# Kernel tuning notes

Hardware: AMD Instinct MI355X
Metric: run time of the kernel (lower is better)

Reference implementation:

```python
import jax, jax.numpy as jnp
import numpy as np

CR = 64                      # cond_repeat
DILS = tuple(2 ** i for _ in range(2) for i in range(10))  # 2 blocks x 10 layers
Q_ZERO = 128


def setup_inputs() -> dict:
    key = jax.random.key(0)
    B, C, TE = 8, 64, 8          # batch, cond channels, encoding timesteps
    R, S, Q = 128, 128, 256      # residual, skip, classes
    L = len(DILS)
    ks = jax.random.split(key, 12)
    sc = 0.1
    return {
        "encodings": jax.random.normal(ks[0], (B, C, TE), jnp.float32),
        "first_w": jax.random.normal(ks[1], (R, 1, 2), jnp.float32) * sc,
        "first_b": jnp.zeros((R,), jnp.float32),
        "causal_w": jax.random.normal(ks[2], (L, 2 * R, R, 2), jnp.float32) * sc,
        "causal_b": jnp.zeros((L, 2 * R), jnp.float32),
        "cond_w": jax.random.normal(ks[3], (L, 2 * R, C), jnp.float32) * sc,
        "cond_b": jnp.zeros((L, 2 * R), jnp.float32),
        "res_w": jax.random.normal(ks[4], (L, R, R), jnp.float32) * sc,
        "res_b": jnp.zeros((L, R), jnp.float32),
        "skip_w": jax.random.normal(ks[5], (L, S, R), jnp.float32) * sc,
        "skip_b": jnp.zeros((L, S), jnp.float32),
        "skipc_w": jax.random.normal(ks[6], (S, R), jnp.float32) * sc,
        "skipc_b": jnp.zeros((S,), jnp.float32),
        "fc_w": jax.random.normal(ks[7], (S, S), jnp.float32) * sc,
        "fc_b": jnp.zeros((S,), jnp.float32),
        "condf_w": jax.random.normal(ks[8], (S, C), jnp.float32) * sc,
        "condf_b": jnp.zeros((S,), jnp.float32),
        "logits_w": jax.random.normal(ks[9], (Q, S), jnp.float32) * sc,
        "logits_b": jnp.zeros((Q,), jnp.float32),
    }


def _generate(encodings, first_w, first_b, causal_w, causal_b, cond_w, cond_b,
              res_w, res_b, skip_w, skip_b, skipc_w, skipc_b, fc_w, fc_b,
              condf_w, condf_b, logits_w, logits_b):
    B = encodings.shape[0]
    R = res_w.shape[1]
    T = encodings.shape[2] * CR

    # ring buffers emulate QueuedConv1d (queue length = dilation, zero-initialized)
    buf_first0 = jnp.zeros((B, 1), jnp.float32)
    bufs0 = tuple(jnp.zeros((B, d, R), jnp.float32) for d in DILS)
    sample0 = jnp.full((B,), Q_ZERO, jnp.int32)

    def step(carry, t):
        sample, buf_first, bufs = carry
        x = sample.astype(jnp.float32) / 255.0 - 0.5                      # [B]
        c = jax.lax.dynamic_index_in_dim(encodings, t // CR, axis=2,
                                         keepdims=False)                  # [B,C]
        # first causal conv (1 -> R, kernel 2): tap0 on delayed sample, tap1 on current
        prev0 = buf_first[:, 0]
        buf_first = buf_first.at[:, 0].set(x)
        res = (prev0[:, None] * first_w[None, :, 0, 0]
               + x[:, None] * first_w[None, :, 0, 1] + first_b)           # [B,R]
        skip = res @ skipc_w.T + skipc_b                                  # [B,S]
        new_bufs = []
        for l, d in enumerate(DILS):
            idx = jnp.mod(t, d)
            prev = jax.lax.dynamic_index_in_dim(bufs[l], idx, axis=1, keepdims=False)
            new_bufs.append(jax.lax.dynamic_update_index_in_dim(bufs[l], res, idx, axis=1))
            z = (prev @ causal_w[l, :, :, 0].T + res @ causal_w[l, :, :, 1].T
                 + causal_b[l] + c @ cond_w[l].T + cond_b[l])             # [B,2R]
            gate, out = jnp.split(z, 2, axis=1)
            h = jax.nn.sigmoid(gate) * jnp.tanh(out)                      # [B,R]
            res = res + h @ res_w[l].T + res_b[l]
            skip = skip + h @ skip_w[l].T + skip_b[l]
        s = jax.nn.relu(skip) @ fc_w.T + fc_b + c @ condf_w.T + condf_b
        logits = jax.nn.relu(s) @ logits_w.T + logits_b                   # [B,Q]
        sample = jnp.argmax(logits, axis=1).astype(jnp.int32)             # 'max' sampling
        return (sample, buf_first, tuple(new_bufs)), (sample, logits)

    _, (samples, logits) = jax.lax.scan(step, (sample0, buf_first0, bufs0),
                                        jnp.arange(T))
    return samples, logits  # [T,B] int32, [T,B,Q] float32


def reference(encodings, first_w, first_b, causal_w, causal_b, cond_w, cond_b,
              res_w, res_b, skip_w, skip_b, skipc_w, skipc_b, fc_w, fc_b,
              condf_w, condf_b, logits_w, logits_b):
    return _generate(encodings, first_w, first_b, causal_w, causal_b, cond_w, cond_b,
                     res_w, res_b, skip_w, skip_b, skipc_w, skipc_b, fc_w, fc_b,
                     condf_w, condf_b, logits_w, logits_b)
```

## Files before the change

### kernel.cpp

```cpp
#include <hip/hip_runtime.h>
#include <math.h>

#define BB 8
#define TT 512
#define LL 20
#define NBLK 64
#define NTHR 256

typedef float f4 __attribute__((ext_vector_type(4)));
typedef unsigned long long ull;

__constant__ int c_dil[LL] = {1,2,4,8,16,32,64,128,256,512,
                              1,2,4,8,16,32,64,128,256,512};
__constant__ int c_roff[LL] = {-1,0,4096,12288,28672,61440,126976,258048,520192,1044480,
                               2093056,2095104,2099200,2107392,2123776,2156544,
                               2222080,2353152,2615296,3139584};

constexpr size_t OFF_RING = 0;
constexpr size_t OFF_X    = 4188160;

#define P_WC     0
#define P_TB     0
#define P_F      20480
#define P_CZ0    30208
#define P_KC     32256
#define P_WST    32512
#define P_WF0    33024
#define P_WF1    33152
#define P_FB     33280
#define P_CONDZ  33408
#define P_SFC    34048
#define P_RESB   34064
#define P_SKIPB  34104
#define P_ZB     34144
#define P_LOGB   34224
#define P_SKC    34228
#define P_XS     34234
#define P_SL     34258
#define P_SKACC  34290
#define P_R2     34306
#define P_CF     34322
#define P_PREVF  34852
#define P_HF     35908
#define P_RESF   38020
#define POOL_FL  40132

__device__ __forceinline__ f4 ldx(const f4* p) {
    f4 r;
    asm volatile("global_load_dwordx4 %0, %1, off sc0 sc1\n\ts_waitcnt vmcnt(0)"
                 : "=v"(r) : "v"(p) : "memory");
    return r;
}
__device__ __forceinline__ void ldx2(const f4* p0, const f4* p1, f4& a, f4& b) {
    asm volatile("global_load_dwordx4 %0, %2, off sc0 sc1\n\t"
                 "global_load_dwordx4 %1, %3, off sc0 sc1\n\t"
                 "s_waitcnt vmcnt(0)"
                 : "=&v"(a), "=&v"(b) : "v"(p0), "v"(p1) : "memory");
}
__device__ __forceinline__ void ld4x(const f4* a0, const f4* a1, const f4* a2, const f4* a3,
                                     f4& r0, f4& r1, f4& r2, f4& r3) {
    asm volatile("global_load_dwordx4 %0, %4, off sc0 sc1\n\t"
                 "global_load_dwordx4 %1, %5, off sc0 sc1\n\t"
                 "global_load_dwordx4 %2, %6, off sc0 sc1\n\t"
                 "global_load_dwordx4 %3, %7, off sc0 sc1\n\t"
                 "s_waitcnt vmcnt(0)"
                 : "=&v"(r0), "=&v"(r1), "=&v"(r2), "=&v"(r3)
                 : "v"(a0), "v"(a1), "v"(a2), "v"(a3) : "memory");
}
__device__ __forceinline__ void stx(f4* p, f4 v) {
    asm volatile("global_store_dwordx4 %0, %1, off sc0 sc1"
                 :: "v"(p), "v"(v) : "memory");
}
__device__ __forceinline__ void spin(const f4* p, int e, f4& a) {
    while (__float_as_int(a.w) != e) a = ldx(p);
}

__device__ __forceinline__ void pub2(f4* slot, int J, int q, float v0, float v1, int e) {
    f4 v; v.x = v0; v.y = v1; v.z = 0.f; v.w = __int_as_float(e);
    stx(slot + J*8 + q, v);
}
__device__ __forceinline__ void scat2(float* dst, f4 v, int idx, bool dorelu) {
    int Jb = idx >> 3, q = idx & 7;
    float x = v.x, y = v.y;
    if (dorelu) { x = fmaxf(x, 0.f); y = fmaxf(y, 0.f); }
    if (q < 4) {
        dst[(2*q)*132 + 2*Jb]     = x;
        dst[(2*q+1)*132 + 2*Jb]   = y;
    } else {
        dst[(2*q-8)*132 + 2*Jb+1] = x;
        dst[(2*q-7)*132 + 2*Jb+1] = y;
    }
}
__device__ __forceinline__ void consume(const f4* slot, int e, float* dst, bool dorelu) {
    int m = threadIdx.x;
    const f4 *p0 = slot + m, *p1 = slot + 256 + m;
    f4 a, b;
    ldx2(p0, p1, a, b);
    spin(p0, e, a);
    spin(p1, e, b);
    scat2(dst, a, m, dorelu);
    scat2(dst, b, m + 256, dorelu);
}
__device__ __forceinline__ void consume_pair(const f4* sR, int eR, float* dR,
                                             const f4* sH, int eH, float* dH) {
    int m = threadIdx.x;
    const f4 *pra = sR + m, *prb = sR + 256 + m, *pha = sH + m, *phb = sH + 256 + m;
    f4 ra, rb, ha, hb;
    ld4x(pra, prb, pha, phb, ra, rb, ha, hb);
    spin(pra, eR, ra);
    spin(prb, eR, rb);
    scat2(dR, ra, m, false);
    scat2(dR, rb, m + 256, false);
    spin(pha, eH, ha);
    spin(phb, eH, hb);
    scat2(dH, ha, m, false);
    scat2(dH, hb, m + 256, false);
}

__global__ __launch_bounds__(NTHR, 1) void wn_gen(
    const float* __restrict__ enc,
    const float* __restrict__ first_w,  const float* __restrict__ first_b,
    const float* __restrict__ causal_w, const float* __restrict__ causal_b,
    const float* __restrict__ cond_w,   const float* __restrict__ cond_b,
    const float* __restrict__ res_w,    const float* __restrict__ res_b,
    const float* __restrict__ skip_w,   const float* __restrict__ skip_b,
    const float* __restrict__ skipc_w,  const float* __restrict__ skipc_b,
    const float* __restrict__ fc_w,     const float* __restrict__ fc_b,
    const float* __restrict__ condf_w,  const float* __restrict__ condf_b,
    const float* __restrict__ logits_w, const float* __restrict__ logits_b,
    float* __restrict__ wsf, float* __restrict__ out)
{
    extern __shared__ float pool[];
    const int tid = threadIdx.x;
    const int J = blockIdx.x;
    float* ring = wsf + OFF_RING;
    f4* xb = (f4*)(wsf + OFF_X);

    for (int m = 1024 + tid; m < 20480; m += NTHR) {
        int l = m >> 10, rem = m & 1023, g = rem >> 8, i = rem & 255;
        int grow = (g < 2) ? (2*J + g) : (128 + 2*J + (g - 2));
        int col = i & 127, k = i >> 7;
        pool[P_WC + m] = causal_w[((size_t)(l*256 + grow)*128 + col)*2 + k];
    }
    if (tid < 128) {
        pool[P_WF0 + tid] = first_w[2*tid];
        pool[P_WF1 + tid] = first_w[2*tid + 1];
        pool[P_FB + tid]  = first_b[tid];
    }
    if (tid < 40) {
        int l = tid >> 1, r = tid & 1;
        pool[P_RESB + tid]  = res_b[l*128 + 2*J + r];
        pool[P_SKIPB + tid] = skip_b[l*128 + 2*J + r];
    }
    if (tid < 4) pool[P_LOGB + tid] = logits_b[4*J + tid];
    if (tid < 8) {
        pool[P_XS + tid]      = 128.f/255.f - 0.5f;
        pool[P_XS + 8 + tid]  = 0.f;
        pool[P_XS + 16 + tid] = 0.f;
    }
    float wl[16], wfc[16];
    {
        int g = (tid >> 3) & 3, k = tid & 7;
        #pragma unroll
        for (int i = 0; i < 16; ++i)
            wl[i] = logits_w[(size_t)(4*J + g)*128 + k + 8*i];
        int r2 = (tid >> 6) & 1;
        #pragma unroll
        for (int i = 0; i < 16; ++i)
            wfc[i] = fc_w[(size_t)(2*J + r2)*128 + k + 8*i];
    }
    __syncthreads();

    for (int l = 0; l < 19; ++l) {
        for (int m = tid; m < 512; m += NTHR) {
            int g = m >> 7, j = m & 127;
            const float* w1 = pool + P_WC + ((l+1)*4 + g)*256 + 128;
            const float* rw = res_w + (size_t)l*128*128 + j;
            float acc = 0.f;
            #pragma unroll 8
            for (int i = 0; i < 128; ++i) acc += w1[i] * rw[(size_t)i*128];
            pool[P_F + (l*4 + g)*128 + j] = acc;
        }
    }
    if (tid < 80) {
        int l = tid >> 2, g = tid & 3;
        float acc = 0.f;
        if (l >= 1) {
            const float* w1 = pool + P_WC + (l*4 + g)*256 + 128;
            for (int i = 0; i < 128; ++i) acc += w1[i] * res_b[(l-1)*128 + i];
        }
        pool[P_ZB + tid] = acc;
    }
    {
        int grow = tid;
        const float* cw0 = causal_w + (size_t)grow*256;
        float u = 0.f, c1 = 0.f, a0 = 0.f, kp = 0.f, kc = 0.f;
        for (int j = 0; j < 128; ++j) {
            float w0 = cw0[2*j], w1 = cw0[2*j + 1];
            float f0 = pool[P_WF0 + j], f1 = pool[P_WF1 + j], fbv = pool[P_FB + j];
            u  += w0*f0;  c1 += w0*f1 + w1*f0;  a0 += w1*f1;
            kp += w0*fbv; kc += w1*fbv;
        }
        pool[P_TB + grow*4 + 0] = u;
        pool[P_TB + grow*4 + 1] = c1;
        pool[P_TB + grow*4 + 2] = a0;
        pool[P_TB + grow*4 + 3] = kp;
        pool[P_KC + grow]       = kc;
    }
    if (tid < 2) {
        const float* wr = skipc_w + (size_t)(2*J + tid)*128;
        float sk = skipc_b[2*J + tid], sa = 0.f, sb = 0.f;
        for (int j = 0; j < 128; ++j) {
            sk += wr[j]*pool[P_FB + j];
            sa += wr[j]*pool[P_WF0 + j];
            sb += wr[j]*pool[P_WF1 + j];
        }
        pool[P_SKC + tid*3 + 0] = sk;
        pool[P_SKC + tid*3 + 1] = sa;
        pool[P_SKC + tid*3 + 2] = sb;
    }
    __syncthreads();

    int e = 0;
    int er_pending = 0;
    int esk = 0;

    const int w = tid >> 6, lane = tid & 63;

    for (int t = 0; t < TT; ++t) {
        if ((t & 63) == 0) {
            int te = t >> 6;
            for (int m = tid; m < 512; m += NTHR) {
                int b = m >> 6, j = m & 63;
                pool[P_CF + b*66 + j] = enc[(size_t)b*512 + j*8 + te];
            }
            __syncthreads();
            for (int m = tid; m < 640; m += NTHR) {
                int l = m >> 5, rem = m & 31, g = rem >> 3, b = rem & 7;
                int grow = (g < 2) ? (2*J + g) : (128 + 2*J + (g - 2));
                float acc = causal_b[l*256 + grow] + cond_b[l*256 + grow]
                          + pool[P_ZB + l*4 + g];
                const float* cw = cond_w + (size_t)(l*256 + grow)*64;
                const float* cf = pool + P_CF + b*66;
                for (int j = 0; j < 64; ++j) acc += cw[j]*cf[j];
                pool[P_CONDZ + l*32 + g*8 + b] = acc;
            }
            {
                int grow = tid;
                float base = pool[P_KC + grow] + causal_b[grow] + cond_b[grow];
                const float* cw = cond_w + (size_t)grow*64;
                for (int b = 0; b < 8; ++b) {
                    const float* cf = pool + P_CF + b*66;
                    float acc = base;
                    for (int j = 0; j < 64; ++j) acc += cw[j]*cf[j];
                    pool[P_CZ0 + grow*8 + b] = acc;
                }
            }
            if (tid < 16) {
                int r = tid >> 3, b = tid & 7, row = 2*J + r;
                float acc = fc_b[row] + condf_b[row];
                const float* cw = condf_w + (size_t)row*64;
                const float* cf = pool + P_CF + b*66;
                for (int j = 0; j < 64; ++j) acc += cw[j]*cf[j];
                pool[P_SFC + r*8 + b] = acc;
            }
            __syncthreads();
        }

        {
            int j = tid & 127, bh2 = tid >> 7;
            float kf = (t >= 1) ? 1.f : 0.f;
            const float* tg = pool + P_TB + j*4;
            const float* to = pool + P_TB + (128 + j)*4;
            #pragma unroll
            for (int bb = 0; bb < 4; ++bb) {
                int b = bh2*4 + bb;
                float x0v = pool[P_XS + b], x1v = pool[P_XS + 8 + b], x2v = pool[P_XS + 16 + b];
                float zg = pool[P_CZ0 + j*8 + b]
                         + x2v*tg[0] + x1v*tg[1] + x0v*tg[2] + kf*tg[3];
                float zo = pool[P_CZ0 + (128 + j)*8 + b]
                         + x2v*to[0] + x1v*to[1] + x0v*to[2] + kf*to[3];
                pool[P_HF + b*132 + j] = (1.f/(1.f + expf(-zg))) * tanhf(zo);
            }
        }
        for (int m = tid; m < 1024; m += NTHR) {
            int b = m >> 7, r = m & 127;
            pool[P_RESF + b*132 + r] =
                pool[P_FB + r] + pool[P_XS + 8 + b]*pool[P_WF0 + r]
                               + pool[P_XS + b]    *pool[P_WF1 + r];
        }
        if (tid < 16) {
            int r = tid >> 3, b = tid & 7;
            float x0v = pool[P_XS + b], x1v = pool[P_XS + 8 + b];
            pool[P_SKACC + r*8 + b] = pool[P_SKC + r*3] + x1v*pool[P_SKC + r*3 + 1]
                                                        + x0v*pool[P_SKC + r*3 + 2];
            int row = 2*J + r;
            pool[P_R2 + r*8 + b] = pool[P_FB + row] + x1v*pool[P_WF0 + row]
                                                    + x0v*pool[P_WF1 + row];
        }

        for (int l = 0; l < LL; ++l) {
            const int par = l & 1;
            int ehh = 0;
            if (l >= 1) {
                ++e; ehh = e;
                const int r = w & 1, bh = w >> 1;
                const int b2 = lane >> 4, half = (lane >> 3) & 1, k = lane & 7;
                const int b = bh*4 + b2, g = half*2 + r;
                const float* wz = pool + P_WC + (l*4 + g)*256;
                const float* fm = pool + P_F + ((l-1)*4 + g)*128;
                const float* pv = pool + P_PREVF + b*132;
                const float* rs = pool + P_RESF + (par^1)*1056 + b*132;
                const float* hh = pool + P_HF + (par^1)*1056 + b*132;
                float acc = 0.f;
                #pragma unroll
                for (int i = 0; i < 16; ++i) {
                    int j = k + 8*i;
                    acc += wz[j]*pv[j] + wz[128 + j]*rs[j] + fm[j]*hh[j];
                }
                acc += __shfl_xor(acc,1); acc += __shfl_xor(acc,2); acc += __shfl_xor(acc,4);
                acc += pool[P_CONDZ + l*32 + g*8 + b];
                float zp = __shfl_xor(acc, 8);
                float zg = half ? zp : acc;
                float zo = half ? acc : zp;
                float h  = (1.f/(1.f + expf(-zg))) * tanhf(zo);
                float hnb = __shfl_xor(h, 16);
                if (half == 0 && k == 0 && (b2 & 1) == 0)
                    pub2(xb + (size_t)(ehh & 3)*512, J,
                         r*4 + bh*2 + (b2 >> 1), h, hnb, ehh);
            }
            float wv0, wv1;
            {
                int r0 = tid >> 7, i0 = tid & 127;
                wv0 = res_w [(size_t)(l*128 + 2*J + r0)*128 + i0];
                wv1 = skip_w[(size_t)(l*128 + 2*J + r0)*128 + i0];
            }
            ull pfa = 0, pfb = 0;
            if (l <= 18) {
                int d = c_dil[l+1];
                if (t >= d) {
                    int slot = (t - d) & (2*d - 1);
                    const float* rp = ring + c_roff[l+1] + (size_t)slot*1024 + tid*4;
                    pfa = __hip_atomic_load((const ull*)rp,     __ATOMIC_RELAXED, __HIP_MEMORY_SCOPE_AGENT);
                    pfb = __hip_atomic_load((const ull*)(rp+2), __ATOMIC_RELAXED, __HIP_MEMORY_SCOPE_AGENT);
                }
            }
            if (l >= 1 && l <= 18) {
                consume_pair(xb + (size_t)(er_pending & 3)*512, er_pending,
                             pool + P_RESF + par*1056,
                             xb + (size_t)(ehh & 3)*512, ehh,
                             pool + P_HF + par*1056);
            } else if (l == 19) {
                consume(xb + (size_t)(ehh & 3)*512, ehh, pool + P_HF + par*1056, false);
            }
            pool[P_WST + tid] = wv0;
            pool[P_WST + 256 + tid] = wv1;
            __syncthreads();
            {
                int b = lane >> 3, k = lane & 7;
                int r = w & 1, isSkip = w >> 1;
                if (isSkip || l <= 18) {
                    const float* wr = pool + P_WST + (isSkip ? 256 : 0) + r*128;
                    const float* hh = pool + P_HF + par*1056 + b*132;
                    float acc = 0.f;
                    #pragma unroll
                    for (int i = 0; i < 16; ++i) { int j = k + 8*i; acc += wr[j]*hh[j]; }
                    acc += __shfl_xor(acc,1); acc += __shfl_xor(acc,2); acc += __shfl_xor(acc,4);
                    if (isSkip) {
                        float v = pool[P_SKACC + r*8 + b] + acc + pool[P_SKIPB + l*2 + r];
                        if (k == 0) pool[P_SKACC + r*8 + b] = v;
                        if (l == 19) {
                            float vnb = __shfl_xor(v, 8);
                            if (k == 0 && !(b & 1))
                                pub2(xb + (size_t)((e+1) & 3)*512, J,
                                     r*4 + (b >> 1), v, vnb, e + 1);
                        }
                    } else {
                        float v = pool[P_R2 + r*8 + b] + acc + pool[P_RESB + l*2 + r];
                        if (k == 0) {
                            pool[P_R2 + r*8 + b] = v;
                            int d = c_dil[l+1];
                            int slot = t & (2*d - 1);
                            float* wp = ring + c_roff[l+1] + (size_t)slot*1024 + b*128 + 2*J + r;
                            __hip_atomic_store(wp, v, __ATOMIC_RELAXED, __HIP_MEMORY_SCOPE_AGENT);
                        }
                        if (l <= 17) {
                            float vnb = __shfl_xor(v, 8);
                            if (k == 0 && !(b & 1))
                                pub2(xb + (size_t)((e+1) & 3)*512, J,
                                     r*4 + (b >> 1), v, vnb, e + 1);
                        }
                    }
                }
            }
            if (l <= 17)      { ++e; er_pending = e; }
            else if (l == 19) { ++e; esk = e; }
            if (l <= 18) {
                int b = tid >> 5, c = (tid & 31)*4;
                union { ull u; float f[2]; } u0, u1;
                u0.u = pfa; u1.u = pfb;
                float* dp = pool + P_PREVF + b*132 + c;
                dp[0] = u0.f[0]; dp[1] = u0.f[1]; dp[2] = u1.f[0]; dp[3] = u1.f[1];
            }
            __syncthreads();
        }

        consume(xb + (size_t)(esk & 3)*512, esk, pool + P_HF, false);
        __syncthreads();
        ++e;
        {
            int b = lane >> 3, k = lane & 7, r = w & 1;
            if (w < 2) {
                const float* sk = pool + P_HF + b*132;
                float acc = 0.f;
                #pragma unroll
                for (int i = 0; i < 16; ++i) { int j = k + 8*i; acc += wfc[i]*fmaxf(sk[j], 0.f); }
                acc += __shfl_xor(acc,1); acc += __shfl_xor(acc,2); acc += __shfl_xor(acc,4);
                float v = acc + pool[P_SFC + r*8 + b];
                float vnb = __shfl_xor(v, 8);
                if (k == 0 && !(b & 1))
                    pub2(xb + (size_t)(e & 3)*512, J, r*4 + (b >> 1), v, vnb, e);
            }
        }
        consume(xb + (size_t)(e & 3)*512, e, pool + P_RESF, true);
        __syncthreads();
        {
            int b = tid >> 5, g = (tid >> 3) & 3, k = tid & 7;
            const float* sv = pool + P_RESF + b*132;
            float acc = 0.f;
            #pragma unroll
            for (int i = 0; i < 16; ++i) { int j = k + 8*i; acc += wl[i]*sv[j]; }
            acc += __shfl_xor(acc,1); acc += __shfl_xor(acc,2); acc += __shfl_xor(acc,4);
            float v = acc + pool[P_LOGB + g];
            float best = (k == 0) ? v : -3.4e38f;
            int bi = 4*J + g;
            { float ov = __shfl_xor(best, 8);  int oi = __shfl_xor(bi, 8);
              if (ov > best || (ov == best && oi < bi)) { best = ov; bi = oi; } }
            { float ov = __shfl_xor(best, 16); int oi = __shfl_xor(bi, 16);
              if (ov > best || (ov == best && oi < bi)) { best = ov; bi = oi; } }
            if (k == 0) out[4096 + ((size_t)(t*BB + b))*256 + 4*J + g] = v;
            if ((tid & 31) == 0) { pool[P_SL + 2*b] = best; pool[P_SL + 2*b + 1] = (float)bi; }
        }
        __syncthreads();
        ++e;
        if (tid < 8) {
            int q = tid;
            float v0, v1;
            if (q < 4) { v0 = pool[P_SL + 4*q];     v1 = pool[P_SL + 4*q + 2]; }
            else       { v0 = pool[P_SL + 4*(q-4) + 1]; v1 = pool[P_SL + 4*(q-4) + 3]; }
            pub2(xb + (size_t)(e & 3)*512, J, q, v0, v1, e);
        }
        consume(xb + (size_t)(e & 3)*512, e, pool + P_HF, false);
        __syncthreads();
        if (tid < 64) {
            int b = tid >> 3, j0 = tid & 7;
            float best = -3.4e38f; float bidx = 0.f;
            #pragma unroll
            for (int k2 = 0; k2 < 8; ++k2) {
                int j = j0*8 + k2;
                float v  = pool[P_HF + b*132 + 2*j];
                float id = pool[P_HF + b*132 + 2*j + 1];
                if (v > best || (v == best && id < bidx)) { best = v; bidx = id; }
            }
            #pragma unroll
            for (int m = 4; m >= 1; m >>= 1) {
                float ov = __shfl_xor(best, m); float oi = __shfl_xor(bidx, m);
                if (ov > best || (ov == best && oi < bidx)) { best = ov; bidx = oi; }
            }
            if (j0 == 0) {
                if (J == 0) out[t*BB + b] = bidx;
                pool[P_XS + 16 + b] = pool[P_XS + 8 + b];
                pool[P_XS + 8 + b]  = pool[P_XS + b];
                pool[P_XS + b]      = bidx*(1.f/255.f) - 0.5f;
            }
        }
        __syncthreads();
    }
}

extern "C" void kernel_launch(void* const* d_in, const int* in_sizes, int n_in,
                              void* d_out, int out_size, void* d_ws, size_t ws_size,
                              hipStream_t stream) {
    const float* enc      = (const float*)d_in[0];
    const float* first_w  = (const float*)d_in[1];
    const float* first_b  = (const float*)d_in[2];
    const float* causal_w = (const float*)d_in[3];
    const float* causal_b = (const float*)d_in[4];
    const float* cond_w   = (const float*)d_in[5];
    const float* cond_b   = (const float*)d_in[6];
    const float* res_w    = (const float*)d_in[7];
    const float* res_b    = (const float*)d_in[8];
    const float* skip_w   = (const float*)d_in[9];
    const float* skip_b   = (const float*)d_in[10];
    const float* skipc_w  = (const float*)d_in[11];
    const float* skipc_b  = (const float*)d_in[12];
    const float* fc_w     = (const float*)d_in[13];
    const float* fc_b     = (const float*)d_in[14];
    const float* condf_w  = (const float*)d_in[15];
    const float* condf_b  = (const float*)d_in[16];
    const float* logits_w = (const float*)d_in[17];
    const float* logits_b = (const float*)d_in[18];

    float* wsf = (float*)d_ws;
    float* out = (float*)d_out;

    wn_gen<<<NBLK, NTHR, POOL_FL*4, stream>>>(
        enc, first_w, first_b, causal_w, causal_b, cond_w, cond_b,
        res_w, res_b, skip_w, skip_b, skipc_w, skipc_b, fc_w, fc_b,
        condf_w, condf_b, logits_w, logits_b, wsf, out);
}
```

Measured before the change: 37.01 ms.

## Double block threads and distribute first-layer gate across blocks via exchange

Raises threads per block from 256 to 512 so each consume and reduction handles one slot per thread, with 16-lane dot products and wider shuffle reductions. The first layer's gated activation is now computed only for the block's own rows and published through the inter-block exchange buffer instead of being computed redundantly for all 256 rows in every block. Logits and fc weights move from registers into shared memory. This adds one more cross-block exchange round per timestep in exchange for less redundant work and more parallel lanes per block.

```diff
diff --git a/kernel.cpp b/kernel.cpp
--- a/kernel.cpp
+++ b/kernel.cpp
@@ -5,7 +5,7 @@
 #define TT 512
 #define LL 20
 #define NBLK 64
-#define NTHR 256
+#define NTHR 512
 
 typedef float f4 __attribute__((ext_vector_type(4)));
 typedef unsigned long long ull;
@@ -20,30 +20,32 @@
 constexpr size_t OFF_X    = 4188160;
 
 #define P_WC     0
-#define P_TB     0
 #define P_F      20480
-#define P_CZ0    30208
-#define P_KC     32256
-#define P_WST    32512
-#define P_WF0    33024
-#define P_WF1    33152
-#define P_FB     33280
-#define P_CONDZ  33408
-#define P_SFC    34048
-#define P_RESB   34064
-#define P_SKIPB  34104
-#define P_ZB     34144
-#define P_LOGB   34224
-#define P_SKC    34228
-#define P_XS     34234
-#define P_SL     34258
-#define P_SKACC  34290
-#define P_R2     34306
-#define P_CF     34322
-#define P_PREVF  34852
-#define P_HF     35908
-#define P_RESF   38020
-#define POOL_FL  40132
+#define P_WST    30208
+#define P_WSKIPC 30720
+#define P_WFC    30976
+#define P_WLOG   31232
+#define P_WF0    31744
+#define P_WF1    31872
+#define P_FB     32000
+#define P_CONDZ  32128
+#define P_SFC    32768
+#define P_RESB   32784
+#define P_SKIPB  32824
+#define P_ZB     32864
+#define P_LOGB   32944
+#define P_SKIPCB 32948
+#define P_Z0C    32950
+#define P_SKC    32974
+#define P_XS     32980
+#define P_SL     33004
+#define P_SKACC  33036
+#define P_R2     33052
+#define P_CF     33068
+#define P_PREVF  33596
+#define P_HF     34652
+#define P_RESF   36764
+#define POOL_FL  38876
 
 __device__ __forceinline__ f4 ldx(const f4* p) {
     f4 r;
@@ -56,16 +58,6 @@
                  "global_load_dwordx4 %1, %3, off sc0 sc1\n\t"
                  "s_waitcnt vmcnt(0)"
                  : "=&v"(a), "=&v"(b) : "v"(p0), "v"(p1) : "memory");
-}
-__device__ __forceinline__ void ld4x(const f4* a0, const f4* a1, const f4* a2, const f4* a3,
-                                     f4& r0, f4& r1, f4& r2, f4& r3) {
-    asm volatile("global_load_dwordx4 %0, %4, off sc0 sc1\n\t"
-                 "global_load_dwordx4 %1, %5, off sc0 sc1\n\t"
-                 "global_load_dwordx4 %2, %6, off sc0 sc1\n\t"
-                 "global_load_dwordx4 %3, %7, off sc0 sc1\n\t"
-                 "s_waitcnt vmcnt(0)"
-                 : "=&v"(r0), "=&v"(r1), "=&v"(r2), "=&v"(r3)
-                 : "v"(a0), "v"(a1), "v"(a2), "v"(a3) : "memory");
 }
 __device__ __forceinline__ void stx(f4* p, f4 v) {
     asm volatile("global_store_dwordx4 %0, %1, off sc0 sc1"
@@ -93,28 +85,21 @@
 }
 __device__ __forceinline__ void consume(const f4* slot, int e, float* dst, bool dorelu) {
     int m = threadIdx.x;
-    const f4 *p0 = slot + m, *p1 = slot + 256 + m;
-    f4 a, b;
-    ldx2(p0, p1, a, b);
+    const f4* p0 = slot + m;
+    f4 a = ldx(p0);
     spin(p0, e, a);
-    spin(p1, e, b);
     scat2(dst, a, m, dorelu);
-    scat2(dst, b, m + 256, dorelu);
 }
 __device__ __forceinline__ void consume_pair(const f4* sR, int eR, float* dR,
                                              const f4* sH, int eH, float* dH) {
     int m = threadIdx.x;
-    const f4 *pra = sR + m, *prb = sR + 256 + m, *pha = sH + m, *phb = sH + 256 + m;
-    f4 ra, rb, ha, hb;
-    ld4x(pra, prb, pha, phb, ra, rb, ha, hb);
-    spin(pra, eR, ra);
-    spin(prb, eR, rb);
+    const f4 *pr = sR + m, *ph = sH + m;
+    f4 ra, ha;
+    ldx2(pr, ph, ra, ha);
+    spin(pr, eR, ra);
     scat2(dR, ra, m, false);
-    scat2(dR, rb, m + 256, false);
-    spin(pha, eH, ha);
-    spin(phb, eH, hb);
+    spin(ph, eH, ha);
     scat2(dH, ha, m, false);
-    scat2(dH, hb, m + 256, false);
 }
 
 __global__ __launch_bounds__(NTHR, 1) void wn_gen(
@@ -136,12 +121,21 @@
     float* ring = wsf + OFF_RING;
     f4* xb = (f4*)(wsf + OFF_X);
 
-    for (int m = 1024 + tid; m < 20480; m += NTHR) {
+    for (int m = tid; m < 20480; m += NTHR) {
         int l = m >> 10, rem = m & 1023, g = rem >> 8, i = rem & 255;
         int grow = (g < 2) ? (2*J + g) : (128 + 2*J + (g - 2));
         int col = i & 127, k = i >> 7;
         pool[P_WC + m] = causal_w[((size_t)(l*256 + grow)*128 + col)*2 + k];
     }
+    if (tid < 256) {
+        int r = tid >> 7, i = tid & 127;
+        pool[P_WSKIPC + tid] = skipc_w[(size_t)(2*J + r)*128 + i];
+        pool[P_WFC + tid]    = fc_w[(size_t)(2*J + r)*128 + i];
+    }
+    {
+        int w2 = tid >> 7, i = tid & 127;
+        pool[P_WLOG + tid] = logits_w[(size_t)(4*J + w2)*128 + i];
+    }
     if (tid < 128) {
         pool[P_WF0 + tid] = first_w[2*tid];
         pool[P_WF1 + tid] = first_w[2*tid + 1];
@@ -153,21 +147,11 @@
         pool[P_SKIPB + tid] = skip_b[l*128 + 2*J + r];
     }
     if (tid < 4) pool[P_LOGB + tid] = logits_b[4*J + tid];
+    if (tid < 2) pool[P_SKIPCB + tid] = skipc_b[2*J + tid];
     if (tid < 8) {
         pool[P_XS + tid]      = 128.f/255.f - 0.5f;
         pool[P_XS + 8 + tid]  = 0.f;
         pool[P_XS + 16 + tid] = 0.f;
-    }
-    float wl[16], wfc[16];
-    {
-        int g = (tid >> 3) & 3, k = tid & 7;
-        #pragma unroll
-        for (int i = 0; i < 16; ++i)
-            wl[i] = logits_w[(size_t)(4*J + g)*128 + k + 8*i];
-        int r2 = (tid >> 6) & 1;
-        #pragma unroll
-        for (int i = 0; i < 16; ++i)
-            wfc[i] = fc_w[(size_t)(2*J + r2)*128 + k + 8*i];
     }
     __syncthreads();
 
@@ -191,25 +175,24 @@
         }
         pool[P_ZB + tid] = acc;
     }
-    {
-        int grow = tid;
-        const float* cw0 = causal_w + (size_t)grow*256;
-        float u = 0.f, c1 = 0.f, a0 = 0.f, kp = 0.f, kc = 0.f;
+    if (tid < 4) {
+        const float* w0 = pool + P_WC + tid*256;
+        const float* w1 = w0 + 128;
+        float kp = 0.f, kc = 0.f, u = 0.f, c1 = 0.f, a0 = 0.f;
         for (int j = 0; j < 128; ++j) {
-            float w0 = cw0[2*j], w1 = cw0[2*j + 1];
             float f0 = pool[P_WF0 + j], f1 = pool[P_WF1 + j], fbv = pool[P_FB + j];
-            u  += w0*f0;  c1 += w0*f1 + w1*f0;  a0 += w1*f1;
-            kp += w0*fbv; kc += w1*fbv;
-        }
-        pool[P_TB + grow*4 + 0] = u;
-        pool[P_TB + grow*4 + 1] = c1;
-        pool[P_TB + grow*4 + 2] = a0;
-        pool[P_TB + grow*4 + 3] = kp;
-        pool[P_KC + grow]       = kc;
+            kp += w0[j]*fbv; kc += w1[j]*fbv;
+            u  += w0[j]*f0;  c1 += w0[j]*f1 + w1[j]*f0;  a0 += w1[j]*f1;
+        }
+        pool[P_Z0C + tid*6 + 0] = kp;
+        pool[P_Z0C + tid*6 + 1] = kc;
+        pool[P_Z0C + tid*6 + 2] = u;
+        pool[P_Z0C + tid*6 + 3] = c1;
+        pool[P_Z0C + tid*6 + 4] = a0;
     }
     if (tid < 2) {
-        const float* wr = skipc_w + (size_t)(2*J + tid)*128;
-        float sk = skipc_b[2*J + tid], sa = 0.f, sb = 0.f;
+        const float* wr = pool + P_WSKIPC + tid*128;
+        float sk = pool[P_SKIPCB + tid], sa = 0.f, sb = 0.f;
         for (int j = 0; j < 128; ++j) {
             sk += wr[j]*pool[P_FB + j];
             sa += wr[j]*pool[P_WF0 + j];
@@ -224,8 +207,6 @@
     int e = 0;
     int er_pending = 0;
     int esk = 0;
-
-    const int w = tid >> 6, lane = tid & 63;
 
     for (int t = 0; t < TT; ++t) {
         if ((t & 63) == 0) {
@@ -245,17 +226,6 @@
                 for (int j = 0; j < 64; ++j) acc += cw[j]*cf[j];
                 pool[P_CONDZ + l*32 + g*8 + b] = acc;
             }
-            {
-                int grow = tid;
-                float base = pool[P_KC + grow] + causal_b[grow] + cond_b[grow];
-                const float* cw = cond_w + (size_t)grow*64;
-                for (int b = 0; b < 8; ++b) {
-                    const float* cf = pool + P_CF + b*66;
-                    float acc = base;
-                    for (int j = 0; j < 64; ++j) acc += cw[j]*cf[j];
-                    pool[P_CZ0 + grow*8 + b] = acc;
-                }
-            }
             if (tid < 16) {
                 int r = tid >> 3, b = tid & 7, row = 2*J + r;
                 float acc = fc_b[row] + condf_b[row];
@@ -267,21 +237,23 @@
             __syncthreads();
         }
 
-        {
-            int j = tid & 127, bh2 = tid >> 7;
-            float kf = (t >= 1) ? 1.f : 0.f;
-            const float* tg = pool + P_TB + j*4;
-            const float* to = pool + P_TB + (128 + j)*4;
-            #pragma unroll
-            for (int bb = 0; bb < 4; ++bb) {
-                int b = bh2*4 + bb;
-                float x0v = pool[P_XS + b], x1v = pool[P_XS + 8 + b], x2v = pool[P_XS + 16 + b];
-                float zg = pool[P_CZ0 + j*8 + b]
-                         + x2v*tg[0] + x1v*tg[1] + x0v*tg[2] + kf*tg[3];
-                float zo = pool[P_CZ0 + (128 + j)*8 + b]
-                         + x2v*to[0] + x1v*to[1] + x0v*to[2] + kf*to[3];
-                pool[P_HF + b*132 + j] = (1.f/(1.f + expf(-zg))) * tanhf(zo);
-            }
+        ++e; const int eh0 = e;
+        if (tid < 16) {
+            int r = tid & 1, b = tid >> 1;
+            float kf  = (t >= 1) ? 1.f : 0.f;
+            float x0v = pool[P_XS + b];
+            float x1v = pool[P_XS + 8 + b];
+            float x2v = pool[P_XS + 16 + b];
+            const float* zc = pool + P_Z0C;
+            int g0 = r, g1 = 2 + r;
+            float zg = kf*zc[g0*6+0] + zc[g0*6+1] + x2v*zc[g0*6+2]
+                     + x1v*zc[g0*6+3] + x0v*zc[g0*6+4] + pool[P_CONDZ + g0*8 + b];
+            float zo = kf*zc[g1*6+0] + zc[g1*6+1] + x2v*zc[g1*6+2]
+                     + x1v*zc[g1*6+3] + x0v*zc[g1*6+4] + pool[P_CONDZ + g1*8 + b];
+            float h0v = (1.f/(1.f + expf(-zg))) * tanhf(zo);
+            float hnb = __shfl_xor(h0v, 2);
+            if (!(b & 1))
+                pub2(xb + (size_t)(eh0 & 3)*512, J, r*4 + (b >> 1), h0v, hnb, eh0);
         }
         for (int m = tid; m < 1024; m += NTHR) {
             int b = m >> 7, r = m & 127;
@@ -301,12 +273,15 @@
 
         for (int l = 0; l < LL; ++l) {
             const int par = l & 1;
-            int ehh = 0;
-            if (l >= 1) {
+            int ehh;
+            if (l == 0) {
+                ehh = eh0;
+            } else {
                 ++e; ehh = e;
-                const int r = w & 1, bh = w >> 1;
-                const int b2 = lane >> 4, half = (lane >> 3) & 1, k = lane & 7;
-                const int b = bh*4 + b2, g = half*2 + r;
+                const int wv_ = tid >> 6, lane = tid & 63;
+                const int r = wv_ & 1, bp = wv_ >> 1;
+                const int half = lane >> 5, b2 = (lane >> 4) & 1, k = lane & 15;
+                const int b = bp*2 + b2, g = half*2 + r;
                 const float* wz = pool + P_WC + (l*4 + g)*256;
                 const float* fm = pool + P_F + ((l-1)*4 + g)*128;
                 const float* pv = pool + P_PREVF + b*132;
@@ -314,63 +289,66 @@
                 const float* hh = pool + P_HF + (par^1)*1056 + b*132;
                 float acc = 0.f;
                 #pragma unroll
-                for (int i = 0; i < 16; ++i) {
-                    int j = k + 8*i;
+                for (int i = 0; i < 8; ++i) {
+                    int j = k + 16*i;
                     acc += wz[j]*pv[j] + wz[128 + j]*rs[j] + fm[j]*hh[j];
                 }
-                acc += __shfl_xor(acc,1); acc += __shfl_xor(acc,2); acc += __shfl_xor(acc,4);
+                acc += __shfl_xor(acc,1); acc += __shfl_xor(acc,2);
+                acc += __shfl_xor(acc,4); acc += __shfl_xor(acc,8);
                 acc += pool[P_CONDZ + l*32 + g*8 + b];
-                float zp = __shfl_xor(acc, 8);
+                float zp = __shfl_xor(acc, 32);
                 float zg = half ? zp : acc;
                 float zo = half ? acc : zp;
                 float h  = (1.f/(1.f + expf(-zg))) * tanhf(zo);
                 float hnb = __shfl_xor(h, 16);
-                if (half == 0 && k == 0 && (b2 & 1) == 0)
-                    pub2(xb + (size_t)(ehh & 3)*512, J,
-                         r*4 + bh*2 + (b2 >> 1), h, hnb, ehh);
-            }
-            float wv0, wv1;
+                if (half == 0 && k == 0 && b2 == 0)
+                    pub2(xb + (size_t)(ehh & 3)*512, J, r*4 + bp, h, hnb, ehh);
+            }
+            float wv0;
             {
-                int r0 = tid >> 7, i0 = tid & 127;
-                wv0 = res_w [(size_t)(l*128 + 2*J + r0)*128 + i0];
-                wv1 = skip_w[(size_t)(l*128 + 2*J + r0)*128 + i0];
-            }
-            ull pfa = 0, pfb = 0;
+                int r0 = (tid >> 7) & 1, i0 = tid & 127;
+                const float* src = (tid < 256) ? res_w : skip_w;
+                wv0 = src[(size_t)(l*128 + 2*J + r0)*128 + i0];
+            }
+            ull pf = 0;
             if (l <= 18) {
                 int d = c_dil[l+1];
                 if (t >= d) {
                     int slot = (t - d) & (2*d - 1);
-                    const float* rp = ring + c_roff[l+1] + (size_t)slot*1024 + tid*4;
-                    pfa = __hip_atomic_load((const ull*)rp,     __ATOMIC_RELAXED, __HIP_MEMORY_SCOPE_AGENT);
-                    pfb = __hip_atomic_load((const ull*)(rp+2), __ATOMIC_RELAXED, __HIP_MEMORY_SCOPE_AGENT);
+                    pf = __hip_atomic_load((const ull*)(ring + c_roff[l+1]
+                             + (size_t)slot*1024 + tid*2),
+                             __ATOMIC_RELAXED, __HIP_MEMORY_SCOPE_AGENT);
                 }
             }
-            if (l >= 1 && l <= 18) {
+            if (l == 0) {
+                consume(xb + (size_t)(ehh & 3)*512, ehh, pool + P_HF, false);
+            } else if (l <= 18) {
                 consume_pair(xb + (size_t)(er_pending & 3)*512, er_pending,
                              pool + P_RESF + par*1056,
                              xb + (size_t)(ehh & 3)*512, ehh,
                              pool + P_HF + par*1056);
-            } else if (l == 19) {
+            } else {
                 consume(xb + (size_t)(ehh & 3)*512, ehh, pool + P_HF + par*1056, false);
             }
             pool[P_WST + tid] = wv0;
-            pool[P_WST + 256 + tid] = wv1;
             __syncthreads();
             {
-                int b = lane >> 3, k = lane & 7;
-                int r = w & 1, isSkip = w >> 1;
-                if (isSkip || l <= 18) {
-                    const float* wr = pool + P_WST + (isSkip ? 256 : 0) + r*128;
+                const int lane = tid & 63, k = lane & 15, bq = lane >> 4;
+                const int w4 = (tid >> 6) & 3, r = w4 & 1, role = tid >> 8;
+                const int b = (w4 >> 1)*4 + bq;
+                if (role == 1 || l <= 18) {
+                    const float* wr = pool + P_WST + role*256 + r*128;
                     const float* hh = pool + P_HF + par*1056 + b*132;
                     float acc = 0.f;
                     #pragma unroll
-                    for (int i = 0; i < 16; ++i) { int j = k + 8*i; acc += wr[j]*hh[j]; }
-                    acc += __shfl_xor(acc,1); acc += __shfl_xor(acc,2); acc += __shfl_xor(acc,4);
-                    if (isSkip) {
+                    for (int i = 0; i < 8; ++i) { int j = k + 16*i; acc += wr[j]*hh[j]; }
+                    acc += __shfl_xor(acc,1); acc += __shfl_xor(acc,2);
+                    acc += __shfl_xor(acc,4); acc += __shfl_xor(acc,8);
+                    if (role == 1) {
                         float v = pool[P_SKACC + r*8 + b] + acc + pool[P_SKIPB + l*2 + r];
                         if (k == 0) pool[P_SKACC + r*8 + b] = v;
                         if (l == 19) {
-                            float vnb = __shfl_xor(v, 8);
+                            float vnb = __shfl_xor(v, 16);
                             if (k == 0 && !(b & 1))
                                 pub2(xb + (size_t)((e+1) & 3)*512, J,
                                      r*4 + (b >> 1), v, vnb, e + 1);
@@ -381,11 +359,12 @@
                             pool[P_R2 + r*8 + b] = v;
                             int d = c_dil[l+1];
                             int slot = t & (2*d - 1);
-                            float* wp = ring + c_roff[l+1] + (size_t)slot*1024 + b*128 + 2*J + r;
-                            __hip_atomic_store(wp, v, __ATOMIC_RELAXED, __HIP_MEMORY_SCOPE_AGENT);
+                            __hip_atomic_store(ring + c_roff[l+1] + (size_t)slot*1024
+                                                   + b*128 + 2*J + r,
+                                               v, __ATOMIC_RELAXED, __HIP_MEMORY_SCOPE_AGENT);
                         }
                         if (l <= 17) {
-                            float vnb = __shfl_xor(v, 8);
+                            float vnb = __shfl_xor(v, 16);
                             if (k == 0 && !(b & 1))
                                 pub2(xb + (size_t)((e+1) & 3)*512, J,
                                      r*4 + (b >> 1), v, vnb, e + 1);
@@ -396,11 +375,10 @@
             if (l <= 17)      { ++e; er_pending = e; }
             else if (l == 19) { ++e; esk = e; }
             if (l <= 18) {
-                int b = tid >> 5, c = (tid & 31)*4;
-                union { ull u; float f[2]; } u0, u1;
-                u0.u = pfa; u1.u = pfb;
-                float* dp = pool + P_PREVF + b*132 + c;
-                dp[0] = u0.f[0]; dp[1] = u0.f[1]; dp[2] = u1.f[0]; dp[3] = u1.f[1];
+                int b = tid >> 6, c = (tid & 63)*2;
+                union { ull u; float f[2]; } u0; u0.u = pf;
+                pool[P_PREVF + b*132 + c]     = u0.f[0];
+                pool[P_PREVF + b*132 + c + 1] = u0.f[1];
             }
             __syncthreads();
         }
@@ -408,45 +386,47 @@
         consume(xb + (size_t)(esk & 3)*512, esk, pool + P_HF, false);
         __syncthreads();
         ++e;
-        {
-            int b = lane >> 3, k = lane & 7, r = w & 1;
-            if (w < 2) {
-                const float* sk = pool + P_HF + b*132;
-                float acc = 0.f;
-                #pragma unroll
-                for (int i = 0; i < 16; ++i) { int j = k + 8*i; acc += wfc[i]*fmaxf(sk[j], 0.f); }
-                acc += __shfl_xor(acc,1); acc += __shfl_xor(acc,2); acc += __shfl_xor(acc,4);
-                float v = acc + pool[P_SFC + r*8 + b];
-                float vnb = __shfl_xor(v, 8);
-                if (k == 0 && !(b & 1))
-                    pub2(xb + (size_t)(e & 3)*512, J, r*4 + (b >> 1), v, vnb, e);
-            }
+        if (tid < 256) {
+            int r = (tid >> 7) & 1, b = (tid >> 4) & 7, k = tid & 15;
+            const float* wr = pool + P_WFC + r*128;
+            const float* sk = pool + P_HF + b*132;
+            float acc = 0.f;
+            #pragma unroll
+            for (int i = 0; i < 8; ++i) { int j = k + 16*i; acc += wr[j]*fmaxf(sk[j], 0.f); }
+            acc += __shfl_xor(acc,1); acc += __shfl_xor(acc,2);
+            acc += __shfl_xor(acc,4); acc += __shfl_xor(acc,8);
+            float v = acc + pool[P_SFC + r*8 + b];
+            float vnb = __shfl_xor(v, 16);
+            if (k == 0 && !(b & 1))
+                pub2(xb + (size_t)(e & 3)*512, J, r*4 + (b >> 1), v, vnb, e);
         }
         consume(xb + (size_t)(e & 3)*512, e, pool + P_RESF, true);
         __syncthreads();
         {
-            int b = tid >> 5, g = (tid >> 3) & 3, k = tid & 7;
+            int b = tid >> 6, g = (tid >> 4) & 3, k = tid & 15;
+            const float* wr = pool + P_WLOG + g*128;
             const float* sv = pool + P_RESF + b*132;
             float acc = 0.f;
             #pragma unroll
-            for (int i = 0; i < 16; ++i) { int j = k + 8*i; acc += wl[i]*sv[j]; }
-            acc += __shfl_xor(acc,1); acc += __shfl_xor(acc,2); acc += __shfl_xor(acc,4);
+            for (int i = 0; i < 8; ++i) { int j = k + 16*i; acc += wr[j]*sv[j]; }
+            acc += __shfl_xor(acc,1); acc += __shfl_xor(acc,2);
+            acc += __shfl_xor(acc,4); acc += __shfl_xor(acc,8);
             float v = acc + pool[P_LOGB + g];
             float best = (k == 0) ? v : -3.4e38f;
             int bi = 4*J + g;
-            { float ov = __shfl_xor(best, 8);  int oi = __shfl_xor(bi, 8);
-              if (ov > best || (ov == best && oi < bi)) { best = ov; bi = oi; } }
             { float ov = __shfl_xor(best, 16); int oi = __shfl_xor(bi, 16);
               if (ov > best || (ov == best && oi < bi)) { best = ov; bi = oi; } }
+            { float ov = __shfl_xor(best, 32); int oi = __shfl_xor(bi, 32);
+              if (ov > best || (ov == best && oi < bi)) { best = ov; bi = oi; } }
             if (k == 0) out[4096 + ((size_t)(t*BB + b))*256 + 4*J + g] = v;
-            if ((tid & 31) == 0) { pool[P_SL + 2*b] = best; pool[P_SL + 2*b + 1] = (float)bi; }
+            if ((tid & 63) == 0) { pool[P_SL + 2*b] = best; pool[P_SL + 2*b + 1] = (float)bi; }
         }
         __syncthreads();
         ++e;
         if (tid < 8) {
             int q = tid;
             float v0, v1;
-            if (q < 4) { v0 = pool[P_SL + 4*q];     v1 = pool[P_SL + 4*q + 2]; }
+            if (q < 4) { v0 = pool[P_SL + 4*q];         v1 = pool[P_SL + 4*q + 2]; }
             else       { v0 = pool[P_SL + 4*(q-4) + 1]; v1 = pool[P_SL + 4*(q-4) + 3]; }
             pub2(xb + (size_t)(e & 3)*512, J, q, v0, v1, e);
         }
```

Result: faster. 36.06 ms (-2.6%).
